# Kernel optimization log

Hardware: AMD Instinct MI355X
Metric: run time of the kernel (lower is better)

The kernel has to match this reference:

```python
import jax, jax.numpy as jnp
import numpy as np

S, B, W, H = 97, 256, 1024, 16
HD = W // H


def setup_inputs() -> dict:
    key = jax.random.key(0)
    ks = jax.random.split(key, 16)
    def p(k, shape):
        return jax.random.normal(k, shape, jnp.float32) * 0.02
    return {
        "tensor": jax.random.normal(ks[0], (S, B, W), jnp.float32),
        "mask": jnp.zeros((S, S), jnp.float32),
        "q_w": p(ks[1], (W, W)), "q_b": p(ks[2], (W,)),
        "k_w": p(ks[3], (W, W)), "k_b": p(ks[4], (W,)),
        "v_w": p(ks[5], (W, W)), "v_b": p(ks[6], (W,)),
        "in_proj_w": p(ks[7], (3 * W, W)), "in_proj_b": p(ks[8], (3 * W,)),
        "mha_out_w": p(ks[9], (W, W)), "mha_out_b": p(ks[10], (W,)),
        "out_w": p(ks[11], (W, W)), "out_b": p(ks[12], (W,)),
    }


def _freqs_cos_sin(dim, seqlen, theta=10000.0):
    # matches precompute_freqs_cis: angle[t, j] = t / theta**(2j/dim)
    inv = 1.0 / (theta ** (jnp.arange(0, dim, 2, dtype=jnp.float32) / dim))  # (dim/2,)
    ang = jnp.arange(seqlen, dtype=jnp.float32)[:, None] * inv[None, :]      # (S, dim/2)
    return jnp.cos(ang)[:, None, :], jnp.sin(ang)[:, None, :]                # (S, 1, dim/2)


def _rotary(x, cos, sin):
    # x: (S, B, D); pairs (even, odd) along last dim form complex numbers
    s, b, d = x.shape
    xr = x.reshape(s, b, d // 2, 2)
    xe, xo = xr[..., 0], xr[..., 1]
    oe = xe * cos - xo * sin
    oo = xe * sin + xo * cos
    return jnp.stack([oe, oo], axis=-1).reshape(s, b, d)


def reference(tensor, mask, q_w, q_b, k_w, k_b, v_w, v_b,
              in_proj_w, in_proj_b, mha_out_w, mha_out_b, out_w, out_b):
    # tensor: (S, B, W) -- torch MHA default batch_first=False layout
    q = tensor @ q_w.T + q_b
    k = tensor @ k_w.T + k_b
    v = tensor @ v_w.T + v_b

    cos, sin = _freqs_cos_sin(W, S)
    q = _rotary(q, cos, sin)
    k = _rotary(k, cos, sin)

    # nn.MultiheadAttention internal in_proj (applied on top of q/k/v linears)
    Wq, Wk, Wv = in_proj_w[:W], in_proj_w[W:2 * W], in_proj_w[2 * W:]
    bq, bk, bv = in_proj_b[:W], in_proj_b[W:2 * W], in_proj_b[2 * W:]
    q = q @ Wq.T + bq
    k = k @ Wk.T + bk
    v = v @ Wv.T + bv

    def split_heads(x):  # (S,B,W) -> (B,H,S,HD)
        return x.reshape(S, B, H, HD).transpose(1, 2, 0, 3)

    qh, kh, vh = split_heads(q), split_heads(k), split_heads(v)
    scale = 1.0 / jnp.sqrt(jnp.float32(HD))
    scores = jnp.einsum('bhqd,bhkd->bhqk', qh, kh) * scale + mask  # additive float mask
    attn = jax.nn.softmax(scores, axis=-1)
    o = jnp.einsum('bhqk,bhkd->bhqd', attn, vh)      # (B,H,S,HD)
    o = o.transpose(2, 0, 1, 3).reshape(S, B, W)     # (S,B,W)
    o = o @ mha_out_w.T + mha_out_b                  # MHA out_proj
    return o @ out_w.T + out_b                       # module's final self.out
```

## Files before the change

kernel.cpp:

```cpp
#include <hip/hip_runtime.h>
#include <cstdint>
#include <cstddef>

#define S_LEN 97
#define B_DIM 256
#define W_DIM 1024
#define NH    16
#define HDIM  64
#define MROWS (S_LEN * B_DIM)

typedef unsigned short u16;
typedef __bf16 bf16x8 __attribute__((ext_vector_type(8)));
typedef float  f32x4  __attribute__((ext_vector_type(4)));

__device__ __forceinline__ u16 f2bf(float f) {
  __bf16 b = (__bf16)f;
  return __builtin_bit_cast(unsigned short, b);
}
__device__ __forceinline__ float bf2f(u16 h) {
  union { uint32_t u; float f; } v; v.u = ((uint32_t)h) << 16;
  return v.f;
}

__device__ __forceinline__ void gload16(const void* g, void* lds) {
  __builtin_amdgcn_global_load_lds(
      (const __attribute__((address_space(1))) void*)(uintptr_t)g,
      (__attribute__((address_space(3))) void*)(uint32_t)(uintptr_t)lds,
      16, 0, 0);
}

__global__ void k_cvt(const float* __restrict__ s, u16* __restrict__ d, int n4) {
  int i = blockIdx.x * blockDim.x + threadIdx.x;
  if (i >= n4) return;
  float4 v = ((const float4*)s)[i];
  uint2 pk;
  pk.x = (uint32_t)f2bf(v.x) | ((uint32_t)f2bf(v.y) << 16);
  pk.y = (uint32_t)f2bf(v.z) | ((uint32_t)f2bf(v.w) << 16);
  ((uint2*)d)[i] = pk;
}

__global__ void k_cvt_t(const float* __restrict__ src, u16* __restrict__ dst) {
  __shared__ float t[32][33];
  const int bx = blockIdx.x * 32, by = blockIdx.y * 32;
  const int tx = threadIdx.x, ty = threadIdx.y;
  for (int yy = ty; yy < 32; yy += 8)
    t[yy][tx] = src[(size_t)(by + yy) * 1024 + bx + tx];
  __syncthreads();
  for (int yy = ty; yy < 32; yy += 8)
    dst[(size_t)(bx + yy) * 1024 + by + tx] = f2bf(t[tx][yy]);
}

__global__ void k_bias2(const float* a, const float* b, float* dst) {
  int i = blockIdx.x * blockDim.x + threadIdx.x;
  if (i >= 2 * W_DIM) return;
  dst[i] = (i < W_DIM) ? a[i] : b[i - W_DIM];
}

__global__ void k_zero(float* dst, int n) {
  int i = blockIdx.x * blockDim.x + threadIdx.x;
  if (i < n) dst[i] = 0.f;
}

__global__ void k_maskpad(const float* __restrict__ mask, float* __restrict__ mp) {
  int i = blockIdx.x * blockDim.x + threadIdx.x;
  int r = i >> 7, c = i & 127;
  float v;
  if (c >= S_LEN) v = -1e30f;
  else if (r < S_LEN) v = mask[r * S_LEN + c];
  else v = 0.f;
  mp[i] = v;
}

__global__ void k_biasfold(const float* __restrict__ M, const float* __restrict__ v,
                           const float* __restrict__ b2, float* __restrict__ out) {
  const int lane = threadIdx.x & 63, wave = threadIdx.x >> 6;
  const int row = blockIdx.x * 4 + wave;
  float s = 0.f;
  for (int k = lane; k < 1024; k += 64) s += M[(size_t)row * 1024 + k] * v[k];
#pragma unroll
  for (int d = 32; d; d >>= 1) s += __shfl_xor(s, d);
  if (lane == 0) out[row] = s + b2[row];
}

__global__ void k_rope_tab(float* __restrict__ tab) {
  int idx = blockIdx.x * blockDim.x + threadIdx.x;
  if (idx >= S_LEN * 512) return;
  int s = idx / 512, i = idx % 512;
  float freq = expf(-(float)i * (9.210340371976184f / 512.0f));
  float ang = (float)s * freq;
  float sv, cv;
  sincosf(ang, &sv, &cv);
  tab[idx * 2 + 0] = cv;
  tab[idx * 2 + 1] = sv;
}

template <int OUT_MODE>
__global__ __launch_bounds__(256) void k_gemm(
    const u16* __restrict__ A, int lda, const u16* __restrict__ Bw,
    const float* __restrict__ bias, void* __restrict__ Cp, int ldc, int K) {
  __shared__ u16 As[128 * 64];
  __shared__ u16 Bs[128 * 64];

  const int tid = threadIdx.x, lane = tid & 63, wave = tid >> 6;
  const int wm = wave >> 1, wn = wave & 1;
  const int m0 = blockIdx.y * 128;
  const int n0 = blockIdx.x * 128;

  f32x4 acc[4][4] = {};

  const int lrow = lane >> 3;
  const int lcol = (lane & 7) * 8;
  const u16* Ag = A + (size_t)(m0 + wave * 8 + lrow) * lda + lcol;
  const u16* Bg = Bw + (size_t)(n0 + wave * 8 + lrow) * K + lcol;
  u16* Asl = As + wave * 8 * 64;
  u16* Bsl = Bs + wave * 8 * 64;

  for (int kt = 0; kt < K; kt += 64) {
#pragma unroll
    for (int i = 0; i < 4; ++i) {
      gload16(Ag + (size_t)(i * 32) * lda + kt, Asl + i * 2048);
      gload16(Bg + (size_t)(i * 32) * K + kt, Bsl + i * 2048);
    }
    __syncthreads();
#pragma unroll
    for (int kk = 0; kk < 2; ++kk) {
      bf16x8 af[4], bfr[4];
#pragma unroll
      for (int m = 0; m < 4; ++m)
        af[m] = *(const bf16x8*)(As + (wm * 64 + m * 16 + (lane & 15)) * 64 + kk * 32 + (lane >> 4) * 8);
#pragma unroll
      for (int n = 0; n < 4; ++n)
        bfr[n] = *(const bf16x8*)(Bs + (wn * 64 + n * 16 + (lane & 15)) * 64 + kk * 32 + (lane >> 4) * 8);
#pragma unroll
      for (int m = 0; m < 4; ++m)
#pragma unroll
        for (int n = 0; n < 4; ++n)
          acc[m][n] = __builtin_amdgcn_mfma_f32_16x16x32_bf16(af[m], bfr[n], acc[m][n], 0, 0, 0);
    }
    __syncthreads();
  }

  const int r0 = (lane >> 4) * 4;
  const int c0 = lane & 15;
#pragma unroll
  for (int m = 0; m < 4; ++m) {
#pragma unroll
    for (int n = 0; n < 4; ++n) {
      const int col = n0 + wn * 64 + n * 16 + c0;
      const float bv = bias[col];
#pragma unroll
      for (int r = 0; r < 4; ++r) {
        const int row = m0 + wm * 64 + m * 16 + r0 + r;
        const float v = acc[m][n][r] + bv;
        if (OUT_MODE == 0) {
          ((u16*)Cp)[(size_t)row * ldc + col] = f2bf(v);
        } else if (OUT_MODE == 2) {
          ((float*)Cp)[(size_t)row * ldc + col] = v;
        }
      }
    }
  }
}

template <int OUT_MODE, int ACOLB, int SCALEQ = 0>
__global__ __launch_bounds__(512, 2) void k_gemm256(
    const u16* __restrict__ A, int lda, const u16* __restrict__ Bw,
    const float* __restrict__ bias, void* __restrict__ Cp, int ldc,
    size_t thirdStride, const float* __restrict__ tab, int Nt) {
  __shared__ u16 lds[3 * 16384];

  const int tid = threadIdx.x, lane = tid & 63, wave = tid >> 6;
  const int wm = wave >> 2, wn = wave & 3;
  const int c0 = lane & 15, hi = lane >> 4;

  const int nwg = gridDim.x;
  const int qq = nwg >> 3, rr_ = nwg & 7;
  const int xcd = blockIdx.x & 7, sub = blockIdx.x >> 3;
  const int seq = (xcd < rr_ ? xcd * (qq + 1) : rr_ * (qq + 1) + (xcd - rr_) * qq) + sub;
  const int mt = seq / Nt, nt = seq - mt * Nt;
  const int m0 = mt * 256, n0 = nt * 256;
  const int aoff = ACOLB ? (n0 & ~1023) : 0;

  const int Lb = tid >> 3, pc = tid & 7;
  const int lcl = pc ^ (Lb & 7);
  const int rsel = lcl >> 2;
  const int csel = (lcl & 3) * 8;
  const u16* aSrc[2]; const u16* bSrc[2];
  uint32_t dOff[2];
#pragma unroll
  for (int rh = 0; rh < 2; ++rh) {
    const int row = 64 * rh + Lb + 128 * rsel;
    aSrc[rh] = A + (size_t)(m0 + row) * lda + aoff + csel;
    bSrc[rh] = Bw + (size_t)(n0 + row) * 1024 + csel;
    dOff[rh] = rh * 4096 + wave * 512;
  }
  auto stageA = [&](int tt, int rh, u16* slot) {
    gload16(aSrc[rh] + tt * 32, slot + dOff[rh]);
  };
  auto stageB = [&](int tt, int rh, u16* slot) {
    gload16(bSrc[rh] + tt * 32, slot + 8192 + dOff[rh]);
  };

  int aofr[8], bofr[4];
#pragma unroll
  for (int m = 0; m < 8; ++m)
    aofr[m] = (m * 16 + c0) * 64 + ((((wm << 2) | hi) ^ (c0 & 7)) * 8);
#pragma unroll
  for (int n = 0; n < 4; ++n)
    bofr[n] = 8192 + ((wn & 1) * 64 + n * 16 + c0) * 64 +
              (((((wn >> 1) << 2) | hi) ^ (c0 & 7)) * 8);

  u16* s0 = lds;
  u16* s1 = lds + 16384;
  u16* s2 = lds + 32768;

  stageA(0, 0, s0); stageA(0, 1, s0); stageB(0, 0, s0); stageB(0, 1, s0);
  stageA(1, 0, s1); stageA(1, 1, s1); stageB(1, 0, s1); stageB(1, 1, s1);
  asm volatile("s_waitcnt vmcnt(4)" ::: "memory");
  __builtin_amdgcn_s_barrier();
  __builtin_amdgcn_sched_barrier(0);

  f32x4 acc[8][4] = {};
  bf16x8 afP[4], afN[4], bfrC[4];
#pragma unroll
  for (int n = 0; n < 4; ++n) bfrC[n] = *(const bf16x8*)(s0 + bofr[n]);
#pragma unroll
  for (int m = 0; m < 4; ++m) afP[m] = *(const bf16x8*)(s0 + aofr[m]);

#define MFMA16(MB, AF, BF)                                                      \
  _Pragma("unroll") for (int m = 0; m < 4; ++m)                                 \
  _Pragma("unroll") for (int n = 0; n < 4; ++n)                                 \
      acc[(MB) + m][n] =                                                        \
          __builtin_amdgcn_mfma_f32_16x16x32_bf16(AF[m], BF[n], acc[(MB) + m][n], 0, 0, 0);

  for (int t = 0; t < 32; ++t) {
    const bool pf = (t < 30);

#pragma unroll
    for (int m = 0; m < 4; ++m) afN[m] = *(const bf16x8*)(s0 + aofr[4 + m]);
    if (pf) { stageA(t + 2, 0, s2); stageA(t + 2, 1, s2); }
    __builtin_amdgcn_s_setprio(1);
    MFMA16(0, afP, bfrC);
    __builtin_amdgcn_s_setprio(0);

    if (pf) { stageB(t + 2, 0, s2); stageB(t + 2, 1, s2); }
    __builtin_amdgcn_s_setprio(1);
    MFMA16(4, afN, bfrC);
    __builtin_amdgcn_s_setprio(0);

    if (t < 31) {
      if (t < 30) asm volatile("s_waitcnt vmcnt(4)" ::: "memory");
      else        asm volatile("s_waitcnt vmcnt(0)" ::: "memory");
      __builtin_amdgcn_s_barrier();
      __builtin_amdgcn_sched_barrier(0);
      u16* tmp = s0; s0 = s1; s1 = s2; s2 = tmp;
#pragma unroll
      for (int n = 0; n < 4; ++n) bfrC[n] = *(const bf16x8*)(s0 + bofr[n]);
#pragma unroll
      for (int m = 0; m < 4; ++m) afP[m] = *(const bf16x8*)(s0 + aofr[m]);
    }
  }
#undef MFMA16

  const int r0 = (lane >> 4) * 4;
#pragma unroll
  for (int m = 0; m < 8; ++m) {
#pragma unroll
    for (int n = 0; n < 4; ++n) {
      const int col = n0 + wn * 64 + n * 16 + c0;
      const float bv = bias[col];
      if (OUT_MODE == 3) {
        const int pairI = (col & 1023) >> 1;
        const float sgn = (col & 1) ? 1.f : -1.f;
#pragma unroll
        for (int r = 0; r < 4; ++r) {
          const int row = m0 + wm * 128 + m * 16 + r0 + r;
          const float v = acc[m][n][r] + bv;
          const float p = __shfl_xor(v, 1);
          const float2 cs = ((const float2*)tab)[(row >> 8) * 512 + pairI];
          ((u16*)Cp)[(size_t)row * ldc + col] = f2bf(v * cs.x + sgn * p * cs.y);
        }
      } else {
#pragma unroll
        for (int r = 0; r < 4; ++r) {
          const int row = m0 + wm * 128 + m * 16 + r0 + r;
          const float v = acc[m][n][r] + bv;
          if (OUT_MODE == 0) {
            ((u16*)Cp)[(size_t)row * ldc + col] = f2bf(v);
          } else if (OUT_MODE == 2) {
            ((float*)Cp)[(size_t)row * ldc + col] = v;
          } else {
            const int which = col >> 10, c = col & 1023;
            const int h = c >> 6, d = c & 63;
            const int s = row >> 8, b = row & 255;
            const float sc = (SCALEQ && which == 0) ? 0.125f : 1.0f;
            ((u16*)Cp)[(size_t)which * thirdStride +
                       (((size_t)(b * NH + h) * S_LEN + s) * HDIM + d)] = f2bf(v * sc);
          }
        }
      }
    }
  }
}

__global__ __launch_bounds__(512, 4) void k_attn(const u16* __restrict__ qkv2,
                                                 const float* __restrict__ maskP,
                                                 u16* __restrict__ O1) {
  __shared__ u16 Vt[80 * 128];
  __shared__ u16 Pb[128 * 128];
  __shared__ float redS[128];

  const size_t TS = (size_t)MROWS * W_DIM;
  const int bh = blockIdx.x, b = bh >> 4, h = bh & 15;
  const int tid = threadIdx.x, lane = tid & 63, wave = tid >> 6;
  const int wm = wave >> 2;
  const int wn = wave & 3;
  const int c0 = lane & 15, hi = lane >> 4;

  const u16* Qg = qkv2 + (size_t)bh * (S_LEN * HDIM);
  const u16* Kg = Qg + TS;
  const u16* Vg = Qg + 2 * TS;

  float mk[4][2][4];
#pragma unroll
  for (int m = 0; m < 4; ++m)
#pragma unroll
    for (int n = 0; n < 2; ++n)
#pragma unroll
      for (int r = 0; r < 4; ++r)
        mk[m][n][r] = maskP[(wm * 64 + m * 16 + hi * 4 + r) * 128 + wn * 32 + n * 16 + c0];

  for (int idx = tid; idx < 1024; idx += 512) {
    const int s = idx >> 3, c = (idx & 7) * 8;
    uint4 vv = make_uint4(0, 0, 0, 0);
    if (s < S_LEN) vv = *(const uint4*)(Vg + (size_t)s * HDIM + c);
    u16 tmp[8];
    *(uint4*)tmp = vv;
#pragma unroll
    for (int j = 0; j < 8; ++j)
      Vt[(c + j) * 128 + (s ^ (j << 3))] = tmp[j];
  }
  if (tid < 128) Vt[64 * 128 + tid] = 0x3F80;

  f32x4 acc[4][2] = {};
#pragma unroll
  for (int kk = 0; kk < 2; ++kk) {
    bf16x8 af[4], bfr[2];
#pragma unroll
    for (int m = 0; m < 4; ++m)
      af[m] = *(const bf16x8*)(Qg + (size_t)(wm * 64 + m * 16 + c0) * HDIM + kk * 32 + hi * 8);
#pragma unroll
    for (int n = 0; n < 2; ++n)
      bfr[n] = *(const bf16x8*)(Kg + (size_t)(wn * 32 + n * 16 + c0) * HDIM + kk * 32 + hi * 8);
#pragma unroll
    for (int m = 0; m < 4; ++m)
#pragma unroll
      for (int n = 0; n < 2; ++n)
        acc[m][n] = __builtin_amdgcn_mfma_f32_16x16x32_bf16(af[m], bfr[n], acc[m][n], 0, 0, 0);
  }

#pragma unroll
  for (int m = 0; m < 4; ++m) {
#pragma unroll
    for (int r = 0; r < 4; ++r) {
      const int row = wm * 64 + m * 16 + hi * 4 + r;
#pragma unroll
      for (int n = 0; n < 2; ++n) {
        const int col = wn * 32 + n * 16 + c0;
        const float e = __expf(acc[m][n][r] + mk[m][n][r]);
        Pb[row * 128 + (col ^ ((row & 7) << 3))] = f2bf(e);
      }
    }
  }
  __syncthreads();

  f32x4 o[4] = {};
  f32x4 osum[4] = {};
#pragma unroll
  for (int kk = 0; kk < 4; ++kk) {
    bf16x8 pa[4], vb, vbs;
#pragma unroll
    for (int m = 0; m < 4; ++m) {
      const int row = wm * 64 + m * 16 + c0;
      pa[m] = *(const bf16x8*)(Pb + row * 128 + ((kk * 32 + hi * 8) ^ ((row & 7) << 3)));
    }
    {
      const int d = wn * 16 + c0;
      vb = *(const bf16x8*)(Vt + d * 128 + ((kk * 32 + hi * 8) ^ ((d & 7) << 3)));
    }
    if (wn == 0) {
      const int ds = 64 + c0;
      vbs = *(const bf16x8*)(Vt + ds * 128 + ((kk * 32 + hi * 8) ^ ((ds & 7) << 3)));
    }
#pragma unroll
    for (int m = 0; m < 4; ++m)
      o[m] = __builtin_amdgcn_mfma_f32_16x16x32_bf16(pa[m], vb, o[m], 0, 0, 0);
    if (wn == 0) {
#pragma unroll
      for (int m = 0; m < 4; ++m)
        osum[m] = __builtin_amdgcn_mfma_f32_16x16x32_bf16(pa[m], vbs, osum[m], 0, 0, 0);
    }
  }

  if (wn == 0 && c0 == 0) {
#pragma unroll
    for (int m = 0; m < 4; ++m)
#pragma unroll
      for (int r = 0; r < 4; ++r)
        redS[wm * 64 + m * 16 + hi * 4 + r] = osum[m][r];
  }
  __syncthreads();

  u16* Ob = Pb;
#pragma unroll
  for (int m = 0; m < 4; ++m)
#pragma unroll
    for (int r = 0; r < 4; ++r) {
      const int row = wm * 64 + m * 16 + hi * 4 + r;
      const float iv = 1.0f / redS[row];
      Ob[row * 80 + wn * 16 + c0] = f2bf(o[m][r] * iv);
    }
  __syncthreads();

  if (tid < 4 * S_LEN) {
    const int row = tid >> 2, q = tid & 3;
    const u16* src = Ob + row * 80 + q * 16;
    uint4 a0 = *(const uint4*)(src);
    uint4 a1 = *(const uint4*)(src + 8);
    u16* dst = O1 + ((size_t)row * B_DIM + b) * W_DIM + h * HDIM + q * 16;
    *(uint4*)dst = a0;
    *(uint4*)(dst + 8) = a1;
  }
}

extern "C" void kernel_launch(void* const* d_in, const int* in_sizes, int n_in,
                              void* d_out, int out_size, void* d_ws, size_t ws_size,
                              hipStream_t stream) {
  (void)in_sizes; (void)n_in; (void)out_size; (void)ws_size;
  const float* tensor    = (const float*)d_in[0];
  const float* mask      = (const float*)d_in[1];
  const float* q_w       = (const float*)d_in[2];
  const float* q_b       = (const float*)d_in[3];
  const float* k_w       = (const float*)d_in[4];
  const float* k_b       = (const float*)d_in[5];
  const float* v_w       = (const float*)d_in[6];
  const float* v_b       = (const float*)d_in[7];
  const float* in_proj_w = (const float*)d_in[8];
  const float* in_proj_b = (const float*)d_in[9];
  const float* mha_w     = (const float*)d_in[10];
  const float* mha_b     = (const float*)d_in[11];
  const float* out_w     = (const float*)d_in[12];
  const float* out_b     = (const float*)d_in[13];

  char* ws = (char*)d_ws;
  size_t off = 0;
  auto alloc = [&](size_t bytes) {
    char* p = ws + off;
    off += (bytes + 255) & ~(size_t)255;
    return p;
  };

  const size_t TS = (size_t)MROWS * W_DIM;

  float* tab = (float*)alloc((size_t)S_LEN * 512 * 2 * sizeof(float));
  float* maskP = (float*)alloc((size_t)128 * 128 * sizeof(float));
  u16* Xbf   = (u16*)alloc(TS * 2);
  u16* qkv1  = (u16*)alloc((size_t)MROWS * 2048 * 2);
  u16* qkv2  = (u16*)alloc(TS * 3 * 2);
  u16* WC1   = (u16*)alloc((size_t)2048 * 1024 * 2);
  u16* W2    = (u16*)alloc((size_t)3072 * 1024 * 2);
  u16* WvT   = (u16*)alloc((size_t)1024 * 1024 * 2);
  u16* WmT   = (u16*)alloc((size_t)1024 * 1024 * 2);
  u16* WO    = (u16*)alloc((size_t)1024 * 1024 * 2);
  u16* WVf   = (u16*)alloc((size_t)1024 * 1024 * 2);
  u16* WFf   = (u16*)alloc((size_t)1024 * 1024 * 2);
  float* bc1 = (float*)alloc(2048 * sizeof(float));
  float* bvf = (float*)alloc(1024 * sizeof(float));
  float* bff = (float*)alloc(1024 * sizeof(float));
  float* zb  = (float*)alloc(1024 * sizeof(float));
  u16* O1 = Xbf;

  k_rope_tab<<<dim3((S_LEN * 512 + 255) / 256), 256, 0, stream>>>(tab);
  k_maskpad<<<dim3(64), 256, 0, stream>>>(mask, maskP);
  k_cvt<<<dim3(MROWS * W_DIM / 4 / 256), 256, 0, stream>>>(tensor, Xbf, MROWS * W_DIM / 4);
  k_cvt<<<dim3(1024), 256, 0, stream>>>(q_w, WC1, 262144);
  k_cvt<<<dim3(1024), 256, 0, stream>>>(k_w, WC1 + 1048576, 262144);
  k_cvt<<<dim3(3072), 256, 0, stream>>>(in_proj_w, W2, 786432);
  k_cvt<<<dim3(1024), 256, 0, stream>>>(out_w, WO, 262144);
  k_cvt_t<<<dim3(32, 32), dim3(32, 8), 0, stream>>>(v_w, WvT);
  k_cvt_t<<<dim3(32, 32), dim3(32, 8), 0, stream>>>(mha_w, WmT);
  k_bias2<<<dim3(8), 256, 0, stream>>>(q_b, k_b, bc1);
  k_zero<<<dim3(4), 256, 0, stream>>>(zb, 1024);
  k_biasfold<<<dim3(256), 256, 0, stream>>>(in_proj_w + (size_t)2048 * 1024, v_b,
                                            in_proj_b + 2048, bvf);
  k_biasfold<<<dim3(256), 256, 0, stream>>>(out_w, mha_b, out_b, bff);

  k_gemm<0><<<dim3(8, 8), 256, 0, stream>>>(
      W2 + (size_t)2048 * 1024, 1024, WvT, zb, WVf, 1024, 1024);
  k_gemm<0><<<dim3(8, 8), 256, 0, stream>>>(
      WO, 1024, WmT, zb, WFf, 1024, 1024);

  k_gemm256<3, 0><<<dim3(97 * 8), 512, 0, stream>>>(
      Xbf, W_DIM, WC1, bc1, qkv1, 2048, 0, tab, 8);

  k_gemm256<1, 0><<<dim3(97 * 4), 512, 0, stream>>>(
      Xbf, W_DIM, WVf, bvf, qkv2 + 2 * TS, 0, TS, nullptr, 4);

  k_gemm256<1, 1, 1><<<dim3(97 * 8), 512, 0, stream>>>(
      qkv1, 2048, W2, in_proj_b, qkv2, 0, TS, nullptr, 8);

  k_attn<<<dim3(B_DIM * NH), 512, 0, stream>>>(qkv2, maskP, O1);

  k_gemm256<2, 0><<<dim3(97 * 4), 512, 0, stream>>>(
      O1, W_DIM, WFf, bff, d_out, W_DIM, 0, nullptr, 4);
}
```

Measured before the change: 585.6 us.

## Merge QK and V projection GEMMs and deepen LDS pipeline to four stages

Fuses the rotary Q/K projection GEMM and the folded V projection GEMM into one launch with 12 column tiles, choosing the weight, bias and output per tile. The GEMM main loop moves from triple to quad buffering: it prefetches three k-steps ahead, unrolls by two with ping-pong fragment registers, and loads the next stage's fragments before the current MFMAs. This aims to cut a launch and tail effects and to hide global-load latency better. In exchange LDS use rises to 128KB per block, which may limit occupancy at 2 blocks per CU, and register pressure goes up.

After: 564.0 us. 3.7% less time.

```diff
diff --git a/kernel.cpp b/kernel.cpp
--- a/kernel.cpp
+++ b/kernel.cpp
@@ -162,12 +162,14 @@
   }
 }
 
-template <int OUT_MODE, int ACOLB, int SCALEQ = 0>
+template <int MODE>
 __global__ __launch_bounds__(512, 2) void k_gemm256(
-    const u16* __restrict__ A, int lda, const u16* __restrict__ Bw,
-    const float* __restrict__ bias, void* __restrict__ Cp, int ldc,
-    size_t thirdStride, const float* __restrict__ tab, int Nt) {
-  __shared__ u16 lds[3 * 16384];
+    const u16* __restrict__ A, int lda,
+    const u16* __restrict__ BwA, const u16* __restrict__ BwB,
+    const float* __restrict__ biasA, const float* __restrict__ biasB,
+    void* __restrict__ CpA, void* __restrict__ CpB, int ldc,
+    size_t thirdStride, const float* __restrict__ tab, int Nt, int NtA) {
+  __shared__ u16 lds[4 * 16384];
 
   const int tid = threadIdx.x, lane = tid & 63, wave = tid >> 6;
   const int wm = wave >> 2, wn = wave & 3;
@@ -177,9 +179,27 @@
   const int qq = nwg >> 3, rr_ = nwg & 7;
   const int xcd = blockIdx.x & 7, sub = blockIdx.x >> 3;
   const int seq = (xcd < rr_ ? xcd * (qq + 1) : rr_ * (qq + 1) + (xcd - rr_) * qq) + sub;
-  const int mt = seq / Nt, nt = seq - mt * Nt;
-  const int m0 = mt * 256, n0 = nt * 256;
-  const int aoff = ACOLB ? (n0 & ~1023) : 0;
+  const int mt = seq / Nt, ntRaw = seq - mt * Nt;
+  const int m0 = mt * 256;
+  bool isV = false;
+  int n0 = ntRaw * 256;
+  const u16* Bbase;
+  const float* bias;
+  if (MODE == 0) {
+    if (ntRaw >= NtA) {
+      isV = true;
+      n0 = (ntRaw - NtA) * 256;
+      Bbase = BwB + (size_t)n0 * 1024;
+      bias = biasB;
+    } else {
+      Bbase = BwA + (size_t)n0 * 1024;
+      bias = biasA;
+    }
+  } else {
+    Bbase = BwA + (size_t)n0 * 1024;
+    bias = biasA;
+  }
+  const int aoff = (MODE == 1) ? (n0 & ~1023) : 0;
 
   const int Lb = tid >> 3, pc = tid & 7;
   const int lcl = pc ^ (Lb & 7);
@@ -191,14 +211,14 @@
   for (int rh = 0; rh < 2; ++rh) {
     const int row = 64 * rh + Lb + 128 * rsel;
     aSrc[rh] = A + (size_t)(m0 + row) * lda + aoff + csel;
-    bSrc[rh] = Bw + (size_t)(n0 + row) * 1024 + csel;
+    bSrc[rh] = Bbase + (size_t)row * 1024 + csel;
     dOff[rh] = rh * 4096 + wave * 512;
   }
-  auto stageA = [&](int tt, int rh, u16* slot) {
-    gload16(aSrc[rh] + tt * 32, slot + dOff[rh]);
-  };
-  auto stageB = [&](int tt, int rh, u16* slot) {
-    gload16(bSrc[rh] + tt * 32, slot + 8192 + dOff[rh]);
+  auto stage = [&](int tt, u16* slot) {
+    gload16(aSrc[0] + tt * 32, slot + dOff[0]);
+    gload16(aSrc[1] + tt * 32, slot + dOff[1]);
+    gload16(bSrc[0] + tt * 32, slot + 8192 + dOff[0]);
+    gload16(bSrc[1] + tt * 32, slot + 8192 + dOff[1]);
   };
 
   int aofr[8], bofr[4];
@@ -213,15 +233,15 @@
   u16* s0 = lds;
   u16* s1 = lds + 16384;
   u16* s2 = lds + 32768;
-
-  stageA(0, 0, s0); stageA(0, 1, s0); stageB(0, 0, s0); stageB(0, 1, s0);
-  stageA(1, 0, s1); stageA(1, 1, s1); stageB(1, 0, s1); stageB(1, 1, s1);
+  u16* s3 = lds + 49152;
+
+  stage(0, s0); stage(1, s1); stage(2, s2);
   asm volatile("s_waitcnt vmcnt(4)" ::: "memory");
   __builtin_amdgcn_s_barrier();
   __builtin_amdgcn_sched_barrier(0);
 
   f32x4 acc[8][4] = {};
-  bf16x8 afP[4], afN[4], bfrC[4];
+  bf16x8 afP[4], afQ[4], bfrC[4], bfrD[4], afN[4];
 #pragma unroll
   for (int n = 0; n < 4; ++n) bfrC[n] = *(const bf16x8*)(s0 + bofr[n]);
 #pragma unroll
@@ -233,33 +253,39 @@
       acc[(MB) + m][n] =                                                        \
           __builtin_amdgcn_mfma_f32_16x16x32_bf16(AF[m], BF[n], acc[(MB) + m][n], 0, 0, 0);
 
-  for (int t = 0; t < 32; ++t) {
-    const bool pf = (t < 30);
-
-#pragma unroll
-    for (int m = 0; m < 4; ++m) afN[m] = *(const bf16x8*)(s0 + aofr[4 + m]);
-    if (pf) { stageA(t + 2, 0, s2); stageA(t + 2, 1, s2); }
-    __builtin_amdgcn_s_setprio(1);
-    MFMA16(0, afP, bfrC);
-    __builtin_amdgcn_s_setprio(0);
-
-    if (pf) { stageB(t + 2, 0, s2); stageB(t + 2, 1, s2); }
-    __builtin_amdgcn_s_setprio(1);
-    MFMA16(4, afN, bfrC);
-    __builtin_amdgcn_s_setprio(0);
-
-    if (t < 31) {
-      if (t < 30) asm volatile("s_waitcnt vmcnt(4)" ::: "memory");
-      else        asm volatile("s_waitcnt vmcnt(0)" ::: "memory");
-      __builtin_amdgcn_s_barrier();
-      __builtin_amdgcn_sched_barrier(0);
-      u16* tmp = s0; s0 = s1; s1 = s2; s2 = tmp;
-#pragma unroll
-      for (int n = 0; n < 4; ++n) bfrC[n] = *(const bf16x8*)(s0 + bofr[n]);
-#pragma unroll
-      for (int m = 0; m < 4; ++m) afP[m] = *(const bf16x8*)(s0 + aofr[m]);
-    }
-  }
+#define BODY(T, AFC, BFC, AFX, BFX, SC, SN, SS)                                 \
+  {                                                                             \
+    _Pragma("unroll") for (int m = 0; m < 4; ++m)                               \
+      afN[m] = *(const bf16x8*)(SC + aofr[4 + m]);                              \
+    if ((T) + 3 < 32) stage((T) + 3, SS);                                       \
+    if ((T) < 31) {                                                             \
+      _Pragma("unroll") for (int n = 0; n < 4; ++n)                             \
+        BFX[n] = *(const bf16x8*)(SN + bofr[n]);                                \
+      _Pragma("unroll") for (int m = 0; m < 4; ++m)                             \
+        AFX[m] = *(const bf16x8*)(SN + aofr[m]);                                \
+    }                                                                           \
+    __builtin_amdgcn_s_setprio(1);                                              \
+    MFMA16(0, AFC, BFC);                                                        \
+    __builtin_amdgcn_s_setprio(0);                                              \
+    __builtin_amdgcn_s_setprio(1);                                              \
+    MFMA16(4, afN, BFC);                                                        \
+    __builtin_amdgcn_s_setprio(0);                                              \
+    if ((T) < 29)       asm volatile("s_waitcnt vmcnt(4)" ::: "memory");        \
+    else if ((T) == 29) asm volatile("s_waitcnt vmcnt(0)" ::: "memory");        \
+    if ((T) < 31) {                                                             \
+      __builtin_amdgcn_s_barrier();                                             \
+      __builtin_amdgcn_sched_barrier(0);                                        \
+    }                                                                           \
+  }
+
+  for (int it = 0; it < 16; ++it) {
+    const int t0v = it * 2;
+    BODY(t0v,     afP, bfrC, afQ, bfrD, s0, s1, s3);
+    BODY(t0v + 1, afQ, bfrD, afP, bfrC, s1, s2, s0);
+    u16* ta = s0; u16* tb = s1;
+    s0 = s2; s1 = s3; s2 = ta; s3 = tb;
+  }
+#undef BODY
 #undef MFMA16
 
   const int r0 = (lane >> 4) * 4;
@@ -269,7 +295,7 @@
     for (int n = 0; n < 4; ++n) {
       const int col = n0 + wn * 64 + n * 16 + c0;
       const float bv = bias[col];
-      if (OUT_MODE == 3) {
+      if (MODE == 0 && !isV) {
         const int pairI = (col & 1023) >> 1;
         const float sgn = (col & 1) ? 1.f : -1.f;
 #pragma unroll
@@ -278,25 +304,34 @@
           const float v = acc[m][n][r] + bv;
           const float p = __shfl_xor(v, 1);
           const float2 cs = ((const float2*)tab)[(row >> 8) * 512 + pairI];
-          ((u16*)Cp)[(size_t)row * ldc + col] = f2bf(v * cs.x + sgn * p * cs.y);
+          ((u16*)CpA)[(size_t)row * ldc + col] = f2bf(v * cs.x + sgn * p * cs.y);
+        }
+      } else if (MODE == 0 && isV) {
+        const int h = (col >> 6) & 15, d = col & 63;
+#pragma unroll
+        for (int r = 0; r < 4; ++r) {
+          const int row = m0 + wm * 128 + m * 16 + r0 + r;
+          const int s = row >> 8, b = row & 255;
+          ((u16*)CpB)[(((size_t)(b * NH + h) * S_LEN + s) * HDIM + d)] =
+              f2bf(acc[m][n][r] + bv);
+        }
+      } else if (MODE == 1) {
+        const int which = col >> 10, c = col & 1023;
+        const int h = c >> 6, d = c & 63;
+        const float sc = (which == 0) ? 0.125f : 1.0f;
+#pragma unroll
+        for (int r = 0; r < 4; ++r) {
+          const int row = m0 + wm * 128 + m * 16 + r0 + r;
+          const int s = row >> 8, b = row & 255;
+          ((u16*)CpA)[(size_t)which * thirdStride +
+                      (((size_t)(b * NH + h) * S_LEN + s) * HDIM + d)] =
+              f2bf((acc[m][n][r] + bv) * sc);
         }
       } else {
 #pragma unroll
         for (int r = 0; r < 4; ++r) {
           const int row = m0 + wm * 128 + m * 16 + r0 + r;
-          const float v = acc[m][n][r] + bv;
-          if (OUT_MODE == 0) {
-            ((u16*)Cp)[(size_t)row * ldc + col] = f2bf(v);
-          } else if (OUT_MODE == 2) {
-            ((float*)Cp)[(size_t)row * ldc + col] = v;
-          } else {
-            const int which = col >> 10, c = col & 1023;
-            const int h = c >> 6, d = c & 63;
-            const int s = row >> 8, b = row & 255;
-            const float sc = (SCALEQ && which == 0) ? 0.125f : 1.0f;
-            ((u16*)Cp)[(size_t)which * thirdStride +
-                       (((size_t)(b * NH + h) * S_LEN + s) * HDIM + d)] = f2bf(v * sc);
-          }
+          ((float*)CpA)[(size_t)row * ldc + col] = acc[m][n][r] + bv;
         }
       }
     }
@@ -500,17 +535,14 @@
   k_gemm<0><<<dim3(8, 8), 256, 0, stream>>>(
       WO, 1024, WmT, zb, WFf, 1024, 1024);
 
-  k_gemm256<3, 0><<<dim3(97 * 8), 512, 0, stream>>>(
-      Xbf, W_DIM, WC1, bc1, qkv1, 2048, 0, tab, 8);
-
-  k_gemm256<1, 0><<<dim3(97 * 4), 512, 0, stream>>>(
-      Xbf, W_DIM, WVf, bvf, qkv2 + 2 * TS, 0, TS, nullptr, 4);
-
-  k_gemm256<1, 1, 1><<<dim3(97 * 8), 512, 0, stream>>>(
-      qkv1, 2048, W2, in_proj_b, qkv2, 0, TS, nullptr, 8);
+  k_gemm256<0><<<dim3(97 * 12), 512, 0, stream>>>(
+      Xbf, W_DIM, WC1, WVf, bc1, bvf, qkv1, qkv2 + 2 * TS, 2048, TS, tab, 12, 8);
+
+  k_gemm256<1><<<dim3(97 * 8), 512, 0, stream>>>(
+      qkv1, 2048, W2, nullptr, in_proj_b, nullptr, qkv2, nullptr, 0, TS, nullptr, 8, 0);
 
   k_attn<<<dim3(B_DIM * NH), 512, 0, stream>>>(qkv2, maskP, O1);
 
-  k_gemm256<2, 0><<<dim3(97 * 4), 512, 0, stream>>>(
-      O1, W_DIM, WFf, bff, d_out, W_DIM, 0, nullptr, 4);
-}
+  k_gemm256<2><<<dim3(97 * 4), 512, 0, stream>>>(
+      O1, W_DIM, WFf, nullptr, bff, nullptr, d_out, nullptr, W_DIM, 0, nullptr, 4, 0);
+}
```
